# Optimization experiments

Hardware: AMD Instinct MI355X
Metric: run time of the kernel (lower is better)

The kernel has to match this reference:

```python
import jax, jax.numpy as jnp
import numpy as np

VOCAB, EMB, SEQ = 10000, 256, 250
BATCH, UNITS = 256, 1024


def setup_inputs() -> dict:
    key = jax.random.key(0)
    ks = jax.random.split(key, 12)
    s = lambda k, shape, scale: jax.random.normal(k, shape, dtype=jnp.float32) * scale
    return {
        "tokens": jax.random.randint(ks[0], (BATCH, SEQ), 0, VOCAB),
        "emb": s(ks[1], (VOCAB, EMB), 1.0),
        "W1": s(ks[2], (EMB, 2 * UNITS), 1.0 / np.sqrt(EMB)),
        "b1": jnp.zeros((2 * UNITS,), jnp.float32),
        "W2": s(ks[3], (2 * UNITS, UNITS), 1.0 / np.sqrt(2 * UNITS)),
        "b2": jnp.zeros((UNITS,), jnp.float32),
        "W3": s(ks[4], (EMB, UNITS), 1.0 / np.sqrt(EMB)),
        "b3": jnp.zeros((UNITS,), jnp.float32),
        "W4": s(ks[5], (EMB, UNITS), 1.0 / np.sqrt(EMB)),
        "b4": jnp.zeros((UNITS,), jnp.float32),
        "W5": s(ks[6], (EMB, UNITS), 1.0 / np.sqrt(EMB)),
        "Wout": s(ks[7], (UNITS, 1), 1.0 / np.sqrt(UNITS)),
        "bout": jnp.zeros((1,), jnp.float32),
        "state0": s(ks[8], (BATCH, UNITS), 1.0),
    }


def reference(tokens, emb, W1, b1, W2, b2, W3, b3, W4, b4, W5, Wout, bout, state0):
    x = emb[tokens]  # [B, T, E]

    def cell(s, x_t):
        r = jax.nn.relu(x_t @ W1 + b1)          # [B, 2U]
        m = jnp.tanh(r @ W2 + b2)               # [B, U]
        forget = m * s
        i = jax.nn.sigmoid(x_t @ W3 + b3)
        g = jnp.tanh(x_t @ W4 + b4)
        y = jax.nn.relu(forget + i * g)
        s_new = jax.nn.relu(jax.nn.relu(x_t @ W5) + y)
        return s_new, None

    s_final, _ = jax.lax.scan(cell, state0, jnp.swapaxes(x, 0, 1))  # scan over T
    return jax.nn.sigmoid(s_final @ Wout + bout)  # [B, 1]
```

## Files before the change

### kernel.cpp

```cpp
#include <hip/hip_runtime.h>
#include <math.h>

typedef _Float16 f16;
typedef _Float16 f16x2 __attribute__((ext_vector_type(2)));
typedef _Float16 f16x4 __attribute__((ext_vector_type(4)));
typedef _Float16 f16x8 __attribute__((ext_vector_type(8)));
typedef float f32x4 __attribute__((ext_vector_type(4)));

#define AS1 __attribute__((address_space(1)))
#define AS3 __attribute__((address_space(3)))

__device__ __forceinline__ void gload_lds16(const void* g, void* l) {
    __builtin_amdgcn_global_load_lds((AS1 void*)(g), (AS3 void*)(l), 16, 0, 0);
}

__device__ __forceinline__ float sigmoid_fast(float v) {
    return __builtin_amdgcn_rcpf(1.f + __builtin_amdgcn_exp2f(-1.44269504f * v));
}
__device__ __forceinline__ float tanh_fast(float v) {
    return 1.f - 2.f * __builtin_amdgcn_rcpf(1.f + __builtin_amdgcn_exp2f(2.88539008f * v));
}

__global__ __launch_bounds__(256) void tpose_kernel(const float* __restrict__ W, f16* __restrict__ Wt,
                                                    int K, int N) {
    __shared__ float T[64][65];
    const int k0 = blockIdx.x * 64, n0 = blockIdx.y * 64;
    const int tid = threadIdx.x;
    const int rr = tid >> 4, cc = (tid & 15) * 4;
#pragma unroll
    for (int p = 0; p < 4; ++p) {
        int k = rr + p * 16;
        float4 v = *(const float4*)&W[(size_t)(k0 + k) * N + n0 + cc];
        T[k][cc] = v.x; T[k][cc + 1] = v.y; T[k][cc + 2] = v.z; T[k][cc + 3] = v.w;
    }
    __syncthreads();
#pragma unroll
    for (int p = 0; p < 4; ++p) {
        int n = rr + p * 16;
        f16x4 h;
        h[0] = (f16)T[cc][n]; h[1] = (f16)T[cc + 1][n];
        h[2] = (f16)T[cc + 2][n]; h[3] = (f16)T[cc + 3][n];
        *(f16x4*)&Wt[(size_t)(n0 + n) * K + k0 + cc] = h;
    }
}

__global__ __launch_bounds__(256) void ecast_kernel(const float* __restrict__ emb, f16* __restrict__ E) {
    int r = blockIdx.x * 4 + (threadIdx.x >> 6);
    int c = (threadIdx.x & 63) * 4;
    float4 v = make_float4(0.f, 0.f, 0.f, 0.f);
    if (r < 10000) v = *(const float4*)&emb[(size_t)r * 256 + c];
    f16x4 h;
    h[0] = (f16)v.x; h[1] = (f16)v.y; h[2] = (f16)v.z; h[3] = (f16)v.w;
    *(f16x4*)&E[(size_t)r * 256 + c] = h;
}

template <int ACT>
__device__ __forceinline__ void cs_write(f16* Cs, const f32x4 (&acc)[4][4], const float* bp,
                                         int wr, int wc, int lo16, int hi4) {
#pragma unroll
    for (int n = 0; n < 4; ++n) {
        int col = wc * 64 + n * 16 + lo16;
        float b = bp ? bp[col] : 0.f;
        int ch = col >> 3, el = col & 7;
#pragma unroll
        for (int m = 0; m < 4; ++m) {
#pragma unroll
            for (int j = 0; j < 4; ++j) {
                int row = wr * 64 + m * 16 + hi4 * 4 + j;
                float v = acc[m][n][j] + b;
                float o = (ACT == 0) ? fmaxf(v, 0.f) : ((ACT == 1) ? sigmoid_fast(v) : tanh_fast(v));
                int sw = ch ^ (row & 15);
                Cs[row * 128 + sw * 8 + el] = (f16)o;
            }
        }
    }
}

template <int MODE>
__global__ __launch_bounds__(256) void gemm_main(
    const f16* __restrict__ A, const f16* __restrict__ Bt, int N, int K, int CT,
    const float* __restrict__ bb1, const float* __restrict__ bb3, const float* __restrict__ bb4,
    f16* __restrict__ O0, f16* __restrict__ O1, f16* __restrict__ O3) {
    __shared__ f16 SM[4 * 128 * 64];
    f16* Cs = SM;
    const int nwg = gridDim.x, orig = blockIdx.x;
    const int q = nwg >> 3, rm = nwg & 7;
    const int xcd = orig & 7, loc = orig >> 3;
    const int wg = (xcd < rm ? xcd * (q + 1) : rm * (q + 1) + (xcd - rm) * q) + loc;
    const int rowT = wg / CT, colT = wg - rowT * CT;
    const int row0 = rowT * 128, col0 = colT * 128;

    const int tid = threadIdx.x;
    const int wave = tid >> 6, lane = tid & 63;
    const int wr = wave >> 1, wc = wave & 1;
    const int lo16 = lane & 15, hi4 = lane >> 4;

    const bool PM = (MODE == 0) && (col0 >= 2048) && (col0 < 4096);

    f32x4 acc[4][4] = {};

    auto stage = [&](int buf, int k0) {
        f16* As = SM + buf * 16384;
        f16* Bs = As + 8192;
#pragma unroll
        for (int it = 0; it < 4; ++it) {
            int c = it * 256 + wave * 64 + lane;
            int r = c >> 3, sl = c & 7;
            int kc = ((sl ^ (r & 7)) << 3);
            int brow = col0 + r;
            if (PM) {
                int qc = col0 - 2048 + r;
                int grp = qc >> 5, q2 = qc & 31;
                brow = (q2 < 16) ? (2048 + grp * 16 + q2) : (3072 + grp * 16 + (q2 - 16));
            }
            gload_lds16(A  + (size_t)(row0 + r) * K + (k0 + kc), &As[c * 8]);
            gload_lds16(Bt + (size_t)brow * K + (k0 + kc), &Bs[c * 8]);
        }
    };

    const int nt = K >> 6;
    stage(0, 0);
    __syncthreads();
    for (int t = 0; t < nt; ++t) {
        if (t + 1 < nt) stage((t + 1) & 1, (t + 1) << 6);
        const f16* As = SM + (t & 1) * 16384;
        const f16* Bs = As + 8192;
#pragma unroll
        for (int kk = 0; kk < 64; kk += 32) {
            const int s0 = (kk >> 3) + hi4;
            const int sw = s0 ^ (lo16 & 7);
            f16x8 af[4], bf[4];
#pragma unroll
            for (int m = 0; m < 4; ++m)
                af[m] = *(const f16x8*)&As[(wr * 64 + m * 16 + lo16) * 64 + (sw << 3)];
#pragma unroll
            for (int n = 0; n < 4; ++n)
                bf[n] = *(const f16x8*)&Bs[(wc * 64 + n * 16 + lo16) * 64 + (sw << 3)];
#pragma unroll
            for (int m = 0; m < 4; ++m)
#pragma unroll
                for (int n = 0; n < 4; ++n)
                    acc[m][n] = __builtin_amdgcn_mfma_f32_16x16x32_f16(af[m], bf[n], acc[m][n], 0, 0, 0);
        }
        __syncthreads();
    }

    if (PM) {
        const int c = (col0 - 2048) >> 7;
#pragma unroll
        for (int pair = 0; pair < 2; ++pair) {
            int colg = 16 * (4 * c + 2 * wc + pair) + lo16;
            float bi = bb3[colg], bg = bb4[colg];
            int colL = wc * 32 + pair * 16 + lo16;
#pragma unroll
            for (int m = 0; m < 4; ++m)
#pragma unroll
                for (int j = 0; j < 4; ++j) {
                    int row = wr * 64 + m * 16 + hi4 * 4 + j;
                    float pi = sigmoid_fast(acc[m][2 * pair][j] + bi);
                    float pg = tanh_fast(acc[m][2 * pair + 1][j] + bg);
                    Cs[row * 64 + 8 * ((colL >> 3) ^ (row & 7)) + (colL & 7)] = (f16)(pi * pg);
                }
        }
        __syncthreads();
        const int pcol0 = (col0 - 2048) >> 1;
#pragma unroll
        for (int it = 0; it < 4; ++it) {
            int idx = it * 256 + tid;
            int row = idx >> 3, ch = idx & 7;
            f16x8 v = *(const f16x8*)&Cs[row * 64 + 8 * (ch ^ (row & 7))];
            *(f16x8*)&O1[(size_t)(row0 + row) * 1024 + pcol0 + ch * 8] = v;
        }
        return;
    }

    f16* Oe; size_t ostr; const float* bp; int act;
    if (MODE == 1)          { Oe = O0 + col0;          ostr = 1024; bp = bb1 + col0;          act = 2; }
    else if (col0 < 2048)   { Oe = O0 + col0;          ostr = 2048; bp = bb1 + col0;          act = 0; }
    else                    { Oe = O3 + (col0 - 4096); ostr = 1024; bp = nullptr;             act = 0; }

    if (act == 0) cs_write<0>(Cs, acc, bp, wr, wc, lo16, hi4);
    else          cs_write<2>(Cs, acc, bp, wr, wc, lo16, hi4);
    __syncthreads();

#pragma unroll
    for (int it = 0; it < 8; ++it) {
        int idx = it * 256 + tid;
        int row = idx >> 4, ch = idx & 15;
        int sw = ch ^ (row & 15);
        f16x8 v = *(const f16x8*)&Cs[row * 128 + sw * 8];
        *(f16x8*)&Oe[(size_t)(row0 + row) * ostr + ch * 8] = v;
    }
}

__global__ __launch_bounds__(64) void scan_slice_kernel(
    const int* __restrict__ tokens, const f16* __restrict__ Mt, const f16* __restrict__ Pt,
    const f16* __restrict__ Ut, const float* __restrict__ state0,
    const float* __restrict__ Wout, float* __restrict__ partial) {
    __shared__ int toks[256];
    const int bid = blockIdx.x;
    const int b = bid >> 3, x = bid & 7;
    const int lane = threadIdx.x;
    for (int t = lane; t < 256; t += 64) toks[t] = (t < 250) ? tokens[b * 250 + t] : 0;
    __syncthreads();

    const int u0 = x * 128 + lane * 2;
    float2 sv = *(const float2*)&state0[(size_t)b * 1024 + u0];
    float s0 = sv.x, s1 = sv.y;

    f16x2 m[16], p[16], u[16];
#pragma unroll
    for (int k = 0; k < 12; ++k) {
        size_t nb = (size_t)toks[k] * 1024 + u0;
        m[k] = *(const f16x2*)&Mt[nb];
        p[k] = *(const f16x2*)&Pt[nb];
        u[k] = *(const f16x2*)&Ut[nb];
    }

    for (int tb = 0; tb < 240; tb += 16) {
#pragma unroll
        for (int k = 0; k < 16; ++k) {
            const int ls = (k + 12) & 15;
            size_t nb = (size_t)toks[tb + k + 12] * 1024 + u0;
            m[ls] = *(const f16x2*)&Mt[nb];
            p[ls] = *(const f16x2*)&Pt[nb];
            u[ls] = *(const f16x2*)&Ut[nb];
            float y0 = fmaxf((float)m[k][0] * s0 + (float)p[k][0], 0.f);
            s0 = fmaxf((float)u[k][0] + y0, 0.f);
            float y1 = fmaxf((float)m[k][1] * s1 + (float)p[k][1], 0.f);
            s1 = fmaxf((float)u[k][1] + y1, 0.f);
        }
    }
#pragma unroll
    for (int k = 0; k < 10; ++k) {
        float y0 = fmaxf((float)m[k][0] * s0 + (float)p[k][0], 0.f);
        s0 = fmaxf((float)u[k][0] + y0, 0.f);
        float y1 = fmaxf((float)m[k][1] * s1 + (float)p[k][1], 0.f);
        s1 = fmaxf((float)u[k][1] + y1, 0.f);
    }

    float2 wv = *(const float2*)&Wout[u0];
    float part = s0 * wv.x + s1 * wv.y;
#pragma unroll
    for (int o = 32; o > 0; o >>= 1) part += __shfl_down(part, o, 64);
    if (lane == 0) partial[bid] = part;
}

__global__ __launch_bounds__(256) void final_kernel(const float* __restrict__ partial,
                                                    const float* __restrict__ bout,
                                                    float* __restrict__ out) {
    int b = threadIdx.x;
    float tot = bout[0];
#pragma unroll
    for (int w = 0; w < 8; ++w) tot += partial[b * 8 + w];
    out[b] = sigmoid_fast(tot);
}

extern "C" void kernel_launch(void* const* d_in, const int* in_sizes, int n_in,
                              void* d_out, int out_size, void* d_ws, size_t ws_size,
                              hipStream_t stream) {
    const int*   tokens = (const int*)  d_in[0];
    const float* emb    = (const float*)d_in[1];
    const float* W1     = (const float*)d_in[2];
    const float* b1     = (const float*)d_in[3];
    const float* W2     = (const float*)d_in[4];
    const float* b2     = (const float*)d_in[5];
    const float* W3     = (const float*)d_in[6];
    const float* b3     = (const float*)d_in[7];
    const float* W4     = (const float*)d_in[8];
    const float* b4     = (const float*)d_in[9];
    const float* W5     = (const float*)d_in[10];
    const float* Wout   = (const float*)d_in[11];
    const float* bout   = (const float*)d_in[12];
    const float* state0 = (const float*)d_in[13];
    float* out = (float*)d_out;

    const int RP = 10112;

    char* ws = (char*)d_ws;
    size_t off = 0;
    auto alloc = [&](size_t bytes) -> void* {
        void* p = ws + off;
        off += (bytes + 255) & ~(size_t)255;
        return p;
    };
    f16* WtQ = (f16*)alloc((size_t)5120 * 256 * 2);
    f16* Wt2 = (f16*)alloc((size_t)1024 * 2048 * 2);
    f16* E   = (f16*)alloc((size_t)RP * 256 * 2);
    f16* Rb  = (f16*)alloc((size_t)RP * 2048 * 2);
    f16* Mt  = (f16*)alloc((size_t)RP * 1024 * 2);
    f16* Pt  = (f16*)alloc((size_t)RP * 1024 * 2);
    f16* Ut  = (f16*)alloc((size_t)RP * 1024 * 2);
    float* partial = (float*)alloc((size_t)2048 * 4);
    (void)ws_size; (void)in_sizes; (void)n_in; (void)out_size;

    tpose_kernel<<<dim3(4, 32),  256, 0, stream>>>(W1, WtQ,               256, 2048);
    tpose_kernel<<<dim3(4, 16),  256, 0, stream>>>(W3, WtQ + 2048 * 256,  256, 1024);
    tpose_kernel<<<dim3(4, 16),  256, 0, stream>>>(W4, WtQ + 3072 * 256,  256, 1024);
    tpose_kernel<<<dim3(4, 16),  256, 0, stream>>>(W5, WtQ + 4096 * 256,  256, 1024);
    tpose_kernel<<<dim3(32, 16), 256, 0, stream>>>(W2, Wt2,              2048, 1024);
    ecast_kernel<<<RP / 4, 256, 0, stream>>>(emb, E);

    gemm_main<0><<<(RP / 128) * (5120 / 128), 256, 0, stream>>>(
        E, WtQ, 5120, 256, 5120 / 128, b1, b3, b4, Rb, Pt, Ut);
    gemm_main<1><<<(RP / 128) * (1024 / 128), 256, 0, stream>>>(
        Rb, Wt2, 1024, 2048, 1024 / 128, b2, nullptr, nullptr, Mt, nullptr, nullptr);

    scan_slice_kernel<<<2048, 64, 0, stream>>>(tokens, Mt, Pt, Ut, state0, Wout, partial);
    final_kernel<<<1, 256, 0, stream>>>(partial, bout, out);
}
```

Before: 175.7 us.

## Enlarge GEMM tiles to 256x256 with 512-thread workgroups

Both feature GEMMs move from 128x128 tiles on 256 threads to 256x256 tiles on 512 threads (8 waves in a 2x4 layout). Each wave now holds 8x4 MFMA accumulators, and the staging, swizzle and epilogue LDS layouts are rescaled to match. Padded rows grow to 10240. The aim is more operand reuse per LDS load and fewer global loads per FLOP. In exchange the grid gets much smaller (only 160 workgroups for the W2 GEMM) and the epilogue uses 128KB of LDS, which may leave CUs idle and lower occupancy.

New measurement: 181.2 us. +3.2%, slower.

```diff
diff --git a/kernel.cpp b/kernel.cpp
--- a/kernel.cpp
+++ b/kernel.cpp
@@ -54,59 +54,37 @@
     *(f16x4*)&E[(size_t)r * 256 + c] = h;
 }
 
-template <int ACT>
-__device__ __forceinline__ void cs_write(f16* Cs, const f32x4 (&acc)[4][4], const float* bp,
-                                         int wr, int wc, int lo16, int hi4) {
-#pragma unroll
-    for (int n = 0; n < 4; ++n) {
-        int col = wc * 64 + n * 16 + lo16;
-        float b = bp ? bp[col] : 0.f;
-        int ch = col >> 3, el = col & 7;
-#pragma unroll
-        for (int m = 0; m < 4; ++m) {
-#pragma unroll
-            for (int j = 0; j < 4; ++j) {
-                int row = wr * 64 + m * 16 + hi4 * 4 + j;
-                float v = acc[m][n][j] + b;
-                float o = (ACT == 0) ? fmaxf(v, 0.f) : ((ACT == 1) ? sigmoid_fast(v) : tanh_fast(v));
-                int sw = ch ^ (row & 15);
-                Cs[row * 128 + sw * 8 + el] = (f16)o;
-            }
-        }
-    }
-}
-
 template <int MODE>
-__global__ __launch_bounds__(256) void gemm_main(
+__global__ __launch_bounds__(512, 2) void gemm_main(
     const f16* __restrict__ A, const f16* __restrict__ Bt, int N, int K, int CT,
     const float* __restrict__ bb1, const float* __restrict__ bb3, const float* __restrict__ bb4,
     f16* __restrict__ O0, f16* __restrict__ O1, f16* __restrict__ O3) {
-    __shared__ f16 SM[4 * 128 * 64];
+    __shared__ __align__(16) f16 SM[65536];
     f16* Cs = SM;
     const int nwg = gridDim.x, orig = blockIdx.x;
     const int q = nwg >> 3, rm = nwg & 7;
     const int xcd = orig & 7, loc = orig >> 3;
     const int wg = (xcd < rm ? xcd * (q + 1) : rm * (q + 1) + (xcd - rm) * q) + loc;
     const int rowT = wg / CT, colT = wg - rowT * CT;
-    const int row0 = rowT * 128, col0 = colT * 128;
+    const int row0 = rowT * 256, col0 = colT * 256;
 
     const int tid = threadIdx.x;
     const int wave = tid >> 6, lane = tid & 63;
-    const int wr = wave >> 1, wc = wave & 1;
+    const int wr = wave >> 2, wc = wave & 3;
     const int lo16 = lane & 15, hi4 = lane >> 4;
 
     const bool PM = (MODE == 0) && (col0 >= 2048) && (col0 < 4096);
 
-    f32x4 acc[4][4] = {};
+    f32x4 acc[8][4] = {};
 
     auto stage = [&](int buf, int k0) {
-        f16* As = SM + buf * 16384;
-        f16* Bs = As + 8192;
+        f16* As = SM + buf * 32768;
+        f16* Bs = As + 16384;
 #pragma unroll
         for (int it = 0; it < 4; ++it) {
-            int c = it * 256 + wave * 64 + lane;
+            int c = it * 512 + tid;
             int r = c >> 3, sl = c & 7;
-            int kc = ((sl ^ (r & 7)) << 3);
+            int kc = (sl ^ (r & 7)) << 3;
             int brow = col0 + r;
             if (PM) {
                 int qc = col0 - 2048 + r;
@@ -123,21 +101,24 @@
     __syncthreads();
     for (int t = 0; t < nt; ++t) {
         if (t + 1 < nt) stage((t + 1) & 1, (t + 1) << 6);
-        const f16* As = SM + (t & 1) * 16384;
-        const f16* Bs = As + 8192;
+        const f16* As = SM + (t & 1) * 32768;
+        const f16* Bs = As + 16384;
 #pragma unroll
         for (int kk = 0; kk < 64; kk += 32) {
             const int s0 = (kk >> 3) + hi4;
-            const int sw = s0 ^ (lo16 & 7);
-            f16x8 af[4], bf[4];
-#pragma unroll
-            for (int m = 0; m < 4; ++m)
-                af[m] = *(const f16x8*)&As[(wr * 64 + m * 16 + lo16) * 64 + (sw << 3)];
-#pragma unroll
-            for (int n = 0; n < 4; ++n)
-                bf[n] = *(const f16x8*)&Bs[(wc * 64 + n * 16 + lo16) * 64 + (sw << 3)];
-#pragma unroll
-            for (int m = 0; m < 4; ++m)
+            f16x8 af[8], bf[4];
+#pragma unroll
+            for (int m = 0; m < 8; ++m) {
+                int row = wr * 128 + m * 16 + lo16;
+                af[m] = *(const f16x8*)&As[row * 64 + ((s0 ^ (row & 7)) << 3)];
+            }
+#pragma unroll
+            for (int n = 0; n < 4; ++n) {
+                int row = wc * 64 + n * 16 + lo16;
+                bf[n] = *(const f16x8*)&Bs[row * 64 + ((s0 ^ (row & 7)) << 3)];
+            }
+#pragma unroll
+            for (int m = 0; m < 8; ++m)
 #pragma unroll
                 for (int n = 0; n < 4; ++n)
                     acc[m][n] = __builtin_amdgcn_mfma_f32_16x16x32_f16(af[m], bf[n], acc[m][n], 0, 0, 0);
@@ -146,29 +127,28 @@
     }
 
     if (PM) {
-        const int c = (col0 - 2048) >> 7;
-#pragma unroll
-        for (int pair = 0; pair < 2; ++pair) {
-            int colg = 16 * (4 * c + 2 * wc + pair) + lo16;
-            float bi = bb3[colg], bg = bb4[colg];
-            int colL = wc * 32 + pair * 16 + lo16;
-#pragma unroll
-            for (int m = 0; m < 4; ++m)
+        const int pcol0 = (col0 - 2048) >> 1;
+#pragma unroll
+        for (int p = 0; p < 2; ++p) {
+            int colP = wc * 32 + p * 16 + lo16;
+            float bi = bb3[pcol0 + colP], bg = bb4[pcol0 + colP];
+            int ch = colP >> 3, el = colP & 7;
+#pragma unroll
+            for (int m = 0; m < 8; ++m)
 #pragma unroll
                 for (int j = 0; j < 4; ++j) {
-                    int row = wr * 64 + m * 16 + hi4 * 4 + j;
-                    float pi = sigmoid_fast(acc[m][2 * pair][j] + bi);
-                    float pg = tanh_fast(acc[m][2 * pair + 1][j] + bg);
-                    Cs[row * 64 + 8 * ((colL >> 3) ^ (row & 7)) + (colL & 7)] = (f16)(pi * pg);
+                    int row = wr * 128 + m * 16 + hi4 * 4 + j;
+                    float pi = sigmoid_fast(acc[m][2 * p][j] + bi);
+                    float pg = tanh_fast(acc[m][2 * p + 1][j] + bg);
+                    Cs[row * 128 + ((ch ^ (row & 15)) << 3) + el] = (f16)(pi * pg);
                 }
         }
         __syncthreads();
-        const int pcol0 = (col0 - 2048) >> 1;
-#pragma unroll
-        for (int it = 0; it < 4; ++it) {
-            int idx = it * 256 + tid;
-            int row = idx >> 3, ch = idx & 7;
-            f16x8 v = *(const f16x8*)&Cs[row * 64 + 8 * (ch ^ (row & 7))];
+#pragma unroll
+        for (int it = 0; it < 8; ++it) {
+            int idx = it * 512 + tid;
+            int row = idx >> 4, ch = idx & 15;
+            f16x8 v = *(const f16x8*)&Cs[row * 128 + ((ch ^ (row & 15)) << 3)];
             *(f16x8*)&O1[(size_t)(row0 + row) * 1024 + pcol0 + ch * 8] = v;
         }
         return;
@@ -179,16 +159,28 @@
     else if (col0 < 2048)   { Oe = O0 + col0;          ostr = 2048; bp = bb1 + col0;          act = 0; }
     else                    { Oe = O3 + (col0 - 4096); ostr = 1024; bp = nullptr;             act = 0; }
 
-    if (act == 0) cs_write<0>(Cs, acc, bp, wr, wc, lo16, hi4);
-    else          cs_write<2>(Cs, acc, bp, wr, wc, lo16, hi4);
+#pragma unroll
+    for (int n = 0; n < 4; ++n) {
+        int col = wc * 64 + n * 16 + lo16;
+        float b = bp ? bp[col] : 0.f;
+        int ch = col >> 3, el = col & 7;
+#pragma unroll
+        for (int m = 0; m < 8; ++m)
+#pragma unroll
+            for (int j = 0; j < 4; ++j) {
+                int row = wr * 128 + m * 16 + hi4 * 4 + j;
+                float v = acc[m][n][j] + b;
+                float o = (act == 2) ? tanh_fast(v) : fmaxf(v, 0.f);
+                Cs[row * 256 + ((ch ^ (row & 31)) << 3) + el] = (f16)o;
+            }
+    }
     __syncthreads();
 
 #pragma unroll
-    for (int it = 0; it < 8; ++it) {
-        int idx = it * 256 + tid;
-        int row = idx >> 4, ch = idx & 15;
-        int sw = ch ^ (row & 15);
-        f16x8 v = *(const f16x8*)&Cs[row * 128 + sw * 8];
+    for (int it = 0; it < 16; ++it) {
+        int idx = it * 512 + tid;
+        int row = idx >> 5, ch = idx & 31;
+        f16x8 v = *(const f16x8*)&Cs[row * 256 + ((ch ^ (row & 31)) << 3)];
         *(f16x8*)&Oe[(size_t)(row0 + row) * ostr + ch * 8] = v;
     }
 }
@@ -275,7 +267,7 @@
     const float* state0 = (const float*)d_in[13];
     float* out = (float*)d_out;
 
-    const int RP = 10112;
+    const int RP = 10240;
 
     char* ws = (char*)d_ws;
     size_t off = 0;
@@ -301,10 +293,10 @@
     tpose_kernel<<<dim3(32, 16), 256, 0, stream>>>(W2, Wt2,              2048, 1024);
     ecast_kernel<<<RP / 4, 256, 0, stream>>>(emb, E);
 
-    gemm_main<0><<<(RP / 128) * (5120 / 128), 256, 0, stream>>>(
-        E, WtQ, 5120, 256, 5120 / 128, b1, b3, b4, Rb, Pt, Ut);
-    gemm_main<1><<<(RP / 128) * (1024 / 128), 256, 0, stream>>>(
-        Rb, Wt2, 1024, 2048, 1024 / 128, b2, nullptr, nullptr, Mt, nullptr, nullptr);
+    gemm_main<0><<<(RP / 256) * (5120 / 256), 512, 0, stream>>>(
+        E, WtQ, 5120, 256, 5120 / 256, b1, b3, b4, Rb, Pt, Ut);
+    gemm_main<1><<<(RP / 256) * (1024 / 256), 512, 0, stream>>>(
+        Rb, Wt2, 1024, 2048, 1024 / 256, b2, nullptr, nullptr, Mt, nullptr, nullptr);
 
     scan_slice_kernel<<<2048, 64, 0, stream>>>(tokens, Mt, Pt, Ut, state0, Wout, partial);
     final_kernel<<<1, 256, 0, stream>>>(partial, bout, out);
```
